# Optimization experiments

Measured on AMD Instinct MI355X. Metric: run time of the kernel, lower is better.

The kernel has to match this reference:

```python
import jax, jax.numpy as jnp
import numpy as np

HID, FFN, E, K = 1024, 4096, 8, 2
CAP_FACTOR = 1.25


def setup_inputs() -> dict:
    key = jax.random.key(0)
    k1, k2, k3, k4 = jax.random.split(key, 4)
    B, T = 4, 2048
    x = jax.random.normal(k1, (B, T, HID), dtype=jnp.float32)
    router_w = jax.random.normal(k2, (E, HID), dtype=jnp.float32) * 0.02
    w1 = jax.random.normal(k3, (E, HID, FFN), dtype=jnp.float32) * 0.02
    w2 = jax.random.normal(k4, (E, FFN, HID), dtype=jnp.float32) * 0.02
    return {"x": x, "router_w": router_w, "w1": w1, "w2": w2}


def reference(x, router_w, w1, w2):
    B, T, H = x.shape
    N = B * T
    x_flat = x.reshape(N, H)
    # capacity per expert (static, shape-derived)
    C = max(1, int(CAP_FACTOR * N / E * K))

    # router (eval mode: no noise)
    logits = x_flat @ router_w.T                      # [N, E]
    probs = jax.nn.softmax(logits, axis=-1)
    top_v, top_i = jax.lax.top_k(probs, K)            # [N, K]
    top_v = top_v / jnp.sum(top_v, axis=-1, keepdims=True)

    out = jnp.zeros_like(x_flat)
    for k in range(K):
        eid = top_i[:, k]                             # [N] expert id per token
        gate = top_v[:, k]                            # [N]
        # position of each token within its expert, in token order
        onehot = jax.nn.one_hot(eid, E, dtype=jnp.int32)          # [N, E]
        pos = jnp.take_along_axis(jnp.cumsum(onehot, axis=0), eid[:, None], axis=1)[:, 0] - 1
        keep = pos < C                                # capacity drop (first C in token order)
        slot = jnp.where(keep, eid * C + pos, E * C)  # dropped tokens -> dump slot

        # dispatch: scatter kept tokens into per-expert capacity buffers
        buf = jnp.zeros((E * C + 1, H), dtype=x.dtype).at[slot].add(
            x_flat * keep[:, None].astype(x.dtype))
        expert_in = buf[: E * C].reshape(E, C, H)     # [E, C, H]

        # per-expert FFN (grouped GEMM -> GELU -> grouped GEMM)
        h = jax.nn.gelu(jnp.einsum('ech,ehf->ecf', expert_in, w1), approximate=False)
        y = jnp.einsum('ecf,efh->ech', h, w2)         # [E, C, H]

        # combine: gather back to token order, mask dropped, apply gate
        tok = y.reshape(E * C, H)[jnp.minimum(slot, E * C - 1)]
        out = out + tok * (gate * keep.astype(x.dtype))[:, None]

    return out.reshape(B, T, H)
```

## Files before the change

### kernel.cpp

```cpp
#include <hip/hip_runtime.h>
#include <hip/hip_bf16.h>
#include <math.h>

#define N_TOK 8192
#define HIDD  1024
#define FFND  4096
#define NE    8
#define CAP   2560
#define TMX   20
#define TMX4  10
#define RMAX  16512

typedef __attribute__((ext_vector_type(4))) float  f32x4;
typedef __attribute__((ext_vector_type(8))) __bf16 bf16x8;

__device__ __forceinline__ unsigned short f2bf(float f) {
    unsigned u = __float_as_uint(f);
    u = (u + 0x7fffu + ((u >> 16) & 1u)) >> 16;
    return (unsigned short)u;
}

__device__ __forceinline__ void gld_lds16(const void* g, void* l) {
    __builtin_amdgcn_global_load_lds(
        (const __attribute__((address_space(1))) unsigned int*)g,
        (__attribute__((address_space(3))) unsigned int*)l, 16, 0, 0);
}

template <int R, int C>
__global__ __launch_bounds__(256) void transpose_cvt(const float* __restrict__ W,
                                                     unsigned short* __restrict__ Wt) {
    __shared__ unsigned short st[64][72];
    int e  = blockIdx.z;
    int r0 = blockIdx.y * 64, c0 = blockIdx.x * 64;
    int tid = threadIdx.x;
    int rb = tid >> 4, cq = tid & 15;
    const float* src = W + ((size_t)e * R + r0) * C + c0;
#pragma unroll
    for (int i = 0; i < 4; i++) {
        int kr = i * 16 + rb;
        float4 v = *reinterpret_cast<const float4*>(src + (size_t)kr * C + cq * 4);
        st[cq * 4 + 0][kr] = f2bf(v.x);
        st[cq * 4 + 1][kr] = f2bf(v.y);
        st[cq * 4 + 2][kr] = f2bf(v.z);
        st[cq * 4 + 3][kr] = f2bf(v.w);
    }
    __syncthreads();
    unsigned short* dst = Wt + ((size_t)e * C + c0) * R + r0;
#pragma unroll
    for (int i = 0; i < 4; i++) {
        int cr = i * 16 + rb;
        uint2 v = *reinterpret_cast<const uint2*>(&st[cr][cq * 4]);
        *reinterpret_cast<uint2*>(dst + (size_t)cr * R + cq * 4) = v;
    }
}

__global__ __launch_bounds__(256) void router_kernel(const float* __restrict__ x,
                                                     const float* __restrict__ rw,
                                                     unsigned short* __restrict__ xbf,
                                                     int* __restrict__ cnt,
                                                     int* __restrict__ tok,
                                                     float* __restrict__ gate) {
    __shared__ float4 rwl[2048];
    __shared__ int   e0s[32], e1s[32];
    __shared__ float g0s[32], g1s[32];
    __shared__ int   baseS[16];

    int tid = threadIdx.x, lane = tid & 63, w = tid >> 6;
    for (int i = tid; i < 2048; i += 256) rwl[i] = reinterpret_cast<const float4*>(rw)[i];
    __syncthreads();

    int tbase = blockIdx.x * 32 + w * 8;
    for (int i = 0; i < 8; i++) {
        int t = tbase + i;
        const float4* xr = reinterpret_cast<const float4*>(x) + (size_t)t * 256;
        float4 xv[4];
#pragma unroll
        for (int c = 0; c < 4; c++) xv[c] = xr[c * 64 + lane];
        uint2* xb = reinterpret_cast<uint2*>(xbf) + (size_t)t * 256;
#pragma unroll
        for (int c = 0; c < 4; c++) {
            uint2 p;
            p.x = (unsigned)f2bf(xv[c].x) | ((unsigned)f2bf(xv[c].y) << 16);
            p.y = (unsigned)f2bf(xv[c].z) | ((unsigned)f2bf(xv[c].w) << 16);
            xb[c * 64 + lane] = p;
        }
        float dot[NE];
#pragma unroll
        for (int e = 0; e < NE; e++) {
            float s = 0.f;
#pragma unroll
            for (int c = 0; c < 4; c++) {
                float4 a = rwl[e * 256 + c * 64 + lane];
                s += xv[c].x * a.x + xv[c].y * a.y + xv[c].z * a.z + xv[c].w * a.w;
            }
            dot[e] = s;
        }
#pragma unroll
        for (int e = 0; e < NE; e++) {
            float v = dot[e];
#pragma unroll
            for (int o = 32; o > 0; o >>= 1) v += __shfl_xor(v, o, 64);
            dot[e] = v;
        }
        if (lane == 0) {
            int e0 = 0; float l0 = dot[0];
#pragma unroll
            for (int e = 1; e < NE; e++) if (dot[e] > l0) { l0 = dot[e]; e0 = e; }
            int e1 = -1; float l1 = -3.4e38f;
#pragma unroll
            for (int e = 0; e < NE; e++) if (e != e0 && dot[e] > l1) { l1 = dot[e]; e1 = e; }
            float g0 = 1.f / (1.f + expf(l1 - l0));
            int j = w * 8 + i;
            e0s[j] = e0; e1s[j] = e1; g0s[j] = g0; g1s[j] = 1.f - g0;
        }
    }
    __syncthreads();

    int e0 = 255, e1 = 255, rank0 = 0, rank1 = 0, slotcnt = 0;
    float g0 = 0.f, g1 = 0.f;
    if (w == 0) {
        if (lane < 32) { e0 = e0s[lane]; e1 = e1s[lane]; g0 = g0s[lane]; g1 = g1s[lane]; }
        unsigned long long lt = (1ull << lane) - 1ull;
#pragma unroll
        for (int ee = 0; ee < NE; ee++) {
            unsigned long long m0 = __ballot(e0 == ee);
            unsigned long long m1 = __ballot(e1 == ee);
            if (e0 == ee) rank0 = (int)__popcll(m0 & lt);
            if (e1 == ee) rank1 = (int)__popcll(m1 & lt);
            if (lane == ee)      slotcnt = (int)__popcll(m0);
            if (lane == NE + ee) slotcnt = (int)__popcll(m1);
        }
        if (lane < 16) baseS[lane] = atomicAdd(&cnt[lane * 16], slotcnt);
    }
    __syncthreads();
    if (w == 0 && lane < 32) {
        int t = blockIdx.x * 32 + lane;
        int p0 = baseS[e0] + rank0;
        if (p0 < CAP) { tok[e0 * CAP + p0] = t; gate[e0 * CAP + p0] = g0; }
        int p1 = baseS[NE + e1] + rank1;
        if (p1 < CAP) { tok[(NE + e1) * CAP + p1] = t; gate[(NE + e1) * CAP + p1] = g1; }
    }
}

template <int KD, int ND, int KS, bool G1>
__global__ __launch_bounds__(512, 1) void ffn_gemm4p(const unsigned short* __restrict__ A,
                                                     const unsigned short* __restrict__ Bw,
                                                     unsigned short* __restrict__ H,
                                                     float* __restrict__ O,
                                                     const int* __restrict__ cntAll,
                                                     const int* __restrict__ tokL,
                                                     const float* __restrict__ gateL) {
    constexpr int TN    = ND / 256;
    constexpr int UNITS = TN * KS;
    constexpr int CH    = 4;
    constexpr int KDS   = KD / KS;
    constexpr int NT    = KDS / 32;
    constexpr int BUFSZ = 32768;

    extern __shared__ __align__(16) char smem[];

    int e = blockIdx.x & 7;
    int i = blockIdx.x >> 3;
    int cnt0 = min(cntAll[e * 16], CAP);
    int cnt1 = min(cntAll[(e + 8) * 16], CAP);
    int tmx0 = (cnt0 + 255) >> 8, tmx1 = (cnt1 + 255) >> 8;
    int tmsum = tmx0 + tmx1;
    if (tmsum == 0) return;
    int per_chunk = tmsum * CH;
    int c = i / per_chunk;
    if (c >= UNITS / CH) return;
    int r = i - c * per_chunk;
    int s, tm, cnt_e;
    if (r < tmx0 * CH) { s = e;     tm = r / CH; r -= tm * CH; cnt_e = cnt0; }
    else { r -= tmx0 * CH; s = e + 8; tm = r / CH; r -= tm * CH; cnt_e = cnt1; }
    int u  = c * CH + r;
    int tn = (KS > 1) ? (u / KS) : u;
    int ks = (KS > 1) ? (u % KS) : 0;

    int off_e = 0;
#pragma unroll
    for (int t = 0; t < 16; t++) off_e += (t < s) ? min(cntAll[t * 16], CAP) : 0;
    const int lbase = s * CAP;

    int tid = threadIdx.x;
    int l = tid & 63, w = tid >> 6;

    int rowi   = w * 16 + (l >> 2);
    int schunk = (((l & 3) ^ ((l >> 3) & 3)) << 4);

    int aoff[2], boff[2];
#pragma unroll
    for (int j = 0; j < 2; j++) {
        int p = tm * 256 + j * 128 + rowi;
        if (G1) {
            int t = tokL[lbase + (p < cnt_e ? p : 0)];
            aoff[j] = t * (KD * 2) + ks * (KDS * 2) + schunk;
        } else {
            aoff[j] = (off_e + p) * (KD * 2) + ks * (KDS * 2) + schunk;
        }
        int nr = e * ND + tn * 256 + j * 128 + rowi;
        boff[j] = nr * (KD * 2) + ks * (KDS * 2) + schunk;
    }
    int dstw = w * 1024;

    const char* Ab = (const char*)A;
    const char* Bb = (const char*)Bw;

    int wm = w >> 2, wn = w & 3;
    int rswz = (((l >> 4) ^ ((l >> 1) & 3)) << 4);
    int aRd = (wm * 128 + (l & 15)) * 64 + rswz;
    int bRd = (wn * 64 + (l & 15)) * 64 + rswz + 16384;

    f32x4 acc[8][4];
#pragma unroll
    for (int m = 0; m < 8; m++)
#pragma unroll
        for (int n = 0; n < 4; n++) acc[m][n] = (f32x4){0.f, 0.f, 0.f, 0.f};

#define STAGE_A4(bb) do { _Pragma("unroll") \
    for (int j = 0; j < 2; j++) { gld_lds16(Ab + aoff[j], smem + (bb) + j * 8192 + dstw); aoff[j] += 64; } } while (0)
#define STAGE_B4(bb) do { _Pragma("unroll") \
    for (int j = 0; j < 2; j++) { gld_lds16(Bb + boff[j], smem + (bb) + 16384 + j * 8192 + dstw); boff[j] += 64; } } while (0)

#pragma unroll
    for (int t = 0; t < 3; t++) { STAGE_A4(t * BUFSZ); STAGE_B4(t * BUFSZ); }
    asm volatile("s_waitcnt vmcnt(8)" ::: "memory");
    __builtin_amdgcn_s_barrier();
    asm volatile("" ::: "memory");

    for (int t = 0; t < NT; t++) {
        const int cb = (t & 3) * BUFSZ;
        const int nb = ((t + 3) & 3) * BUFSZ;
        bool pf = (t + 3) < NT;
        bf16x8 af[4], bf[4];
#pragma unroll
        for (int n = 0; n < 4; n++) bf[n] = *reinterpret_cast<const bf16x8*>(smem + cb + bRd + n * 1024);
#pragma unroll
        for (int m = 0; m < 4; m++) af[m] = *reinterpret_cast<const bf16x8*>(smem + cb + aRd + m * 1024);
        if (pf) STAGE_A4(nb);
        __builtin_amdgcn_s_barrier();
        asm volatile("" ::: "memory");
        asm volatile("s_waitcnt lgkmcnt(0)" ::: "memory");
        __builtin_amdgcn_sched_barrier(0);
        __builtin_amdgcn_s_setprio(1);
#pragma unroll
        for (int m = 0; m < 4; m++)
#pragma unroll
            for (int n = 0; n < 4; n++)
                acc[m][n] = __builtin_amdgcn_mfma_f32_16x16x32_bf16(af[m], bf[n], acc[m][n], 0, 0, 0);
        __builtin_amdgcn_s_setprio(0);
        __builtin_amdgcn_s_barrier();
        asm volatile("" ::: "memory");
#pragma unroll
        for (int m = 0; m < 4; m++) af[m] = *reinterpret_cast<const bf16x8*>(smem + cb + aRd + (m + 4) * 1024);
        if (pf) STAGE_B4(nb);
        if (t + 3 < NT)      asm volatile("s_waitcnt vmcnt(8)" ::: "memory");
        else if (t + 2 < NT) asm volatile("s_waitcnt vmcnt(4)" ::: "memory");
        else if (t + 1 < NT) asm volatile("s_waitcnt vmcnt(0)" ::: "memory");
        __builtin_amdgcn_s_barrier();
        asm volatile("" ::: "memory");
        asm volatile("s_waitcnt lgkmcnt(0)" ::: "memory");
        __builtin_amdgcn_sched_barrier(0);
        __builtin_amdgcn_s_setprio(1);
#pragma unroll
        for (int m = 0; m < 4; m++)
#pragma unroll
            for (int n = 0; n < 4; n++)
                acc[m + 4][n] = __builtin_amdgcn_mfma_f32_16x16x32_bf16(af[m], bf[n], acc[m + 4][n], 0, 0, 0);
        __builtin_amdgcn_s_setprio(0);
        __builtin_amdgcn_s_barrier();
        asm volatile("" ::: "memory");
    }
#undef STAGE_A4
#undef STAGE_B4

    if (G1) {
#pragma unroll
        for (int m = 0; m < 8; m++) {
#pragma unroll
            for (int j = 0; j < 4; j++) {
                int rr = wm * 128 + m * 16 + (l >> 4) * 4 + j;
                int p = tm * 256 + rr;
                if (p < cnt_e) {
                    unsigned short* hp = H + (size_t)(off_e + p) * ND + tn * 256 + wn * 64 + (l & 15);
#pragma unroll
                    for (int n = 0; n < 4; n++) {
                        float v = acc[m][n][j];
                        float g = 0.5f * v * (1.f + erff(v * 0.70710678118654752f));
                        hp[n * 16] = f2bf(g);
                    }
                }
            }
        }
    } else {
#pragma unroll
        for (int m = 0; m < 8; m++) {
#pragma unroll
            for (int j = 0; j < 4; j++) {
                int rr = wm * 128 + m * 16 + (l >> 4) * 4 + j;
                int p = tm * 256 + rr;
                if (p < cnt_e) {
                    int t = tokL[lbase + p];
                    float gv = gateL[lbase + p];
                    float* op = O + (size_t)t * ND + tn * 256 + wn * 64 + (l & 15);
#pragma unroll
                    for (int n = 0; n < 4; n++) atomicAdd(op + n * 16, gv * acc[m][n][j]);
                }
            }
        }
    }
}

template <int KD, int ND, bool G1>
__global__ __launch_bounds__(256) void ffn_gemm(const unsigned short* __restrict__ A,
                                                const float* __restrict__ W,
                                                unsigned short* __restrict__ H,
                                                float* __restrict__ O,
                                                const int* __restrict__ cntAll,
                                                const int* __restrict__ tokL,
                                                const float* __restrict__ gateL,
                                                int slot0, int pbase) {
    constexpr int TN = ND / 128;
    int bid = blockIdx.x;
    int tn  = bid % TN;
    int tme = bid / TN;
    int tm  = tme % TMX;
    int s   = slot0 + tme / TMX;
    int eW  = s & 7;
    int cnt_e = min(cntAll[s * 16], CAP);
    if (tm * 128 >= cnt_e) return;
    int off_e = 0;
#pragma unroll
    for (int i = 0; i < 16; i++) {
        int c = min(cntAll[i * 16], CAP);
        off_e += (i >= pbase && i < s) ? c : 0;
    }
    const int lbase = s * CAP;

    __shared__ __align__(16) unsigned short At[128 * 32];
    __shared__ __align__(16) unsigned short Bt[128 * 32];

    int tid = threadIdx.x;
    int w = tid >> 6, l = tid & 63;
    int wr = w >> 1, wc = w & 1;

    int r1 = tid >> 2, q1 = tid & 3;
    int r2 = r1 + 64;
    const char* aSrc1;
    const char* aSrc2;
    if (G1) {
        int p1 = tm * 128 + r1, p2 = tm * 128 + r2;
        int t1 = tokL[lbase + (p1 < cnt_e ? p1 : 0)];
        int t2 = tokL[lbase + (p2 < cnt_e ? p2 : 0)];
        aSrc1 = (const char*)(A + (size_t)t1 * KD) + ((q1 ^ ((r1 >> 1) & 3)) << 4);
        aSrc2 = (const char*)(A + (size_t)t2 * KD) + ((q1 ^ ((r2 >> 1) & 3)) << 4);
    } else {
        size_t row1 = (size_t)off_e + tm * 128 + r1;
        size_t row2 = row1 + 64;
        aSrc1 = (const char*)(A + row1 * KD) + ((q1 ^ ((r1 >> 1) & 3)) << 4);
        aSrc2 = (const char*)(A + row2 * KD) + ((q1 ^ ((r2 >> 1) & 3)) << 4);
    }
    char* aDst1 = (char*)At + w * 1024;
    char* aDst2 = aDst1 + 4096;

    const float* bSrc[4];
    int bOff[16];
#pragma unroll
    for (int j = 0; j < 4; j++) {
        int fidx = j * 1024 + tid * 4;
        int kk = fidx >> 7, n = fidx & 127;
        bSrc[j] = W + (size_t)eW * KD * ND + (size_t)kk * ND + tn * 128 + n;
#pragma unroll
        for (int i = 0; i < 4; i++) {
            int nn = n + i;
            bOff[j * 4 + i] = nn * 64 + ((((kk >> 3) ^ ((nn >> 1) & 3))) << 4) + ((kk & 7) << 1);
        }
    }

    int aro[4], bro[4];
#pragma unroll
    for (int m = 0; m < 4; m++) {
        int rr = wr * 64 + m * 16 + (l & 15);
        aro[m] = rr * 64 + (((l >> 4) ^ ((rr >> 1) & 3)) << 4);
        int cc = wc * 64 + m * 16 + (l & 15);
        bro[m] = cc * 64 + (((l >> 4) ^ ((cc >> 1) & 3)) << 4);
    }

    f32x4 zf = {0.f, 0.f, 0.f, 0.f};
    f32x4 acc[4][4];
#pragma unroll
    for (int m = 0; m < 4; m++)
#pragma unroll
        for (int n = 0; n < 4; n++) acc[m][n] = zf;

    for (int k0 = 0; k0 < KD; k0 += 32) {
        gld_lds16(aSrc1 + (size_t)k0 * 2, aDst1);
        gld_lds16(aSrc2 + (size_t)k0 * 2, aDst2);
        float4 bv[4];
#pragma unroll
        for (int j = 0; j < 4; j++) bv[j] = *reinterpret_cast<const float4*>(bSrc[j] + (size_t)k0 * ND);
        char* btc = (char*)Bt;
#pragma unroll
        for (int j = 0; j < 4; j++) {
            *(unsigned short*)(btc + bOff[j * 4 + 0]) = f2bf(bv[j].x);
            *(unsigned short*)(btc + bOff[j * 4 + 1]) = f2bf(bv[j].y);
            *(unsigned short*)(btc + bOff[j * 4 + 2]) = f2bf(bv[j].z);
            *(unsigned short*)(btc + bOff[j * 4 + 3]) = f2bf(bv[j].w);
        }
        __syncthreads();
        bf16x8 af[4], bf[4];
#pragma unroll
        for (int m = 0; m < 4; m++) af[m] = *reinterpret_cast<const bf16x8*>((const char*)At + aro[m]);
#pragma unroll
        for (int n = 0; n < 4; n++) bf[n] = *reinterpret_cast<const bf16x8*>((const char*)Bt + bro[n]);
#pragma unroll
        for (int m = 0; m < 4; m++)
#pragma unroll
            for (int n = 0; n < 4; n++)
                acc[m][n] = __builtin_amdgcn_mfma_f32_16x16x32_bf16(af[m], bf[n], acc[m][n], 0, 0, 0);
        __syncthreads();
    }

    if (G1) {
#pragma unroll
        for (int m = 0; m < 4; m++) {
#pragma unroll
            for (int j = 0; j < 4; j++) {
                int rr = wr * 64 + m * 16 + (l >> 4) * 4 + j;
                int p = tm * 128 + rr;
                if (p < cnt_e) {
                    size_t row = (size_t)(off_e + p);
                    unsigned short* hp = H + row * ND + tn * 128 + wc * 64 + (l & 15);
#pragma unroll
                    for (int n = 0; n < 4; n++) {
                        float v = acc[m][n][j];
                        float g = 0.5f * v * (1.f + erff(v * 0.70710678118654752f));
                        hp[n * 16] = f2bf(g);
                    }
                }
            }
        }
    } else {
#pragma unroll
        for (int m = 0; m < 4; m++) {
#pragma unroll
            for (int j = 0; j < 4; j++) {
                int rr = wr * 64 + m * 16 + (l >> 4) * 4 + j;
                int p = tm * 128 + rr;
                if (p < cnt_e) {
                    int t = tokL[lbase + p];
                    float gv = gateL[lbase + p];
                    float* op = O + (size_t)t * ND + tn * 128 + wc * 64 + (l & 15);
#pragma unroll
                    for (int n = 0; n < 4; n++) atomicAdd(op + n * 16, gv * acc[m][n][j]);
                }
            }
        }
    }
}

extern "C" void kernel_launch(void* const* d_in, const int* in_sizes, int n_in,
                              void* d_out, int out_size, void* d_ws, size_t ws_size,
                              hipStream_t stream) {
    const float* x  = (const float*)d_in[0];
    const float* rw = (const float*)d_in[1];
    const float* w1 = (const float*)d_in[2];
    const float* w2 = (const float*)d_in[3];
    float* out = (float*)d_out;
    char* ws = (char*)d_ws;

    int*   cnt  = (int*)ws;
    int*   tok  = (int*)(ws + 4096);
    float* gate = (float*)(ws + 4096 + 16 * CAP * 4);
    unsigned short* xbf = (unsigned short*)(ws + (1 << 20));
    size_t hOff = (1 << 20) + (size_t)N_TOK * HIDD * 2;
    unsigned short* h = (unsigned short*)(ws + hOff);

    size_t w1tSz = (size_t)NE * HIDD * FFND * 2;
    size_t hBig = (size_t)RMAX * FFND * 2;
    size_t needBig = hOff + hBig + 2 * w1tSz;

    hipMemsetAsync(cnt, 0, 1024, stream);
    hipMemsetAsync(d_out, 0, (size_t)N_TOK * HIDD * 4, stream);

    hipLaunchKernelGGL(router_kernel, dim3(N_TOK / 32), dim3(256), 0, stream,
                       x, rw, xbf, cnt, tok, gate);

    if (ws_size >= needBig) {
        unsigned short* w1t = (unsigned short*)(ws + hOff + hBig);
        unsigned short* w2t = (unsigned short*)(ws + hOff + hBig + w1tSz);
        hipLaunchKernelGGL((transpose_cvt<HIDD, FFND>), dim3(FFND / 64, HIDD / 64, NE), dim3(256), 0, stream, w1, w1t);
        hipLaunchKernelGGL((transpose_cvt<FFND, HIDD>), dim3(HIDD / 64, FFND / 64, NE), dim3(256), 0, stream, w2, w2t);
        constexpr int SMEM = 4 * 32768;
        hipLaunchKernelGGL((ffn_gemm4p<HIDD, FFND, 1, true>), dim3(8 * 2 * TMX4 * 16), dim3(512),
                           SMEM, stream, xbf, w1t, h, (float*)nullptr, cnt, tok, gate);
        hipLaunchKernelGGL((ffn_gemm4p<FFND, HIDD, 2, false>), dim3(8 * 2 * TMX4 * 8), dim3(512),
                           SMEM, stream, h, w2t, (unsigned short*)nullptr, out, cnt, tok, gate);
    } else {
        for (int k = 0; k < 2; k++) {
            hipLaunchKernelGGL((ffn_gemm<HIDD, FFND, true>), dim3(8 * TMX * (FFND / 128)), dim3(256), 0, stream,
                               xbf, w1, h, (float*)nullptr, cnt, tok, gate, 8 * k, 8 * k);
            hipLaunchKernelGGL((ffn_gemm<FFND, HIDD, false>), dim3(8 * TMX * (HIDD / 128)), dim3(256), 0, stream,
                               h, w2, (unsigned short*)nullptr, out, cnt, tok, gate, 8 * k, 8 * k);
        }
    }
}
```

Measured before the change: 604.4 us.

## Make expert GEMMs persistent with BK=64 tiles and split A/B staging rings

Replaces the one-tile-per-block grid with a persistent grid of 256 blocks, each looping over its expert's tiles with stride 32. The K step doubles to 64 and uses new LDS swizzles. Staging is split into a triple-buffered A ring and a double-buffered B ring, with loads interleaved across four MFMA phases. The aim is to cut launch and tail overhead and halve loop and barrier count per K element. In exchange LDS grows to 160KB per block, and the static stride-32 tile split can leave blocks unevenly loaded.

Result: faster. 558.9 us (-7.5%).

```diff
diff --git a/kernel.cpp b/kernel.cpp
--- a/kernel.cpp
+++ b/kernel.cpp
@@ -8,7 +8,6 @@
 #define NE    8
 #define CAP   2560
 #define TMX   20
-#define TMX4  10
 #define RMAX  16512
 
 typedef __attribute__((ext_vector_type(4))) float  f32x4;
@@ -143,7 +142,7 @@
 }
 
 template <int KD, int ND, int KS, bool G1>
-__global__ __launch_bounds__(512, 1) void ffn_gemm4p(const unsigned short* __restrict__ A,
+__global__ __launch_bounds__(512, 1) void ffn_gemm_t(const unsigned short* __restrict__ A_,
                                                      const unsigned short* __restrict__ Bw,
                                                      unsigned short* __restrict__ H,
                                                      float* __restrict__ O,
@@ -151,164 +150,222 @@
                                                      const int* __restrict__ tokL,
                                                      const float* __restrict__ gateL) {
     constexpr int TN    = ND / 256;
-    constexpr int UNITS = TN * KS;
-    constexpr int CH    = 4;
+    constexpr int TNKS  = TN * KS;
     constexpr int KDS   = KD / KS;
-    constexpr int NT    = KDS / 32;
-    constexpr int BUFSZ = 32768;
+    constexpr int NT    = KDS / 64;
+    constexpr int ABUF  = 32768;
+    constexpr int BBASE = 3 * ABUF;
+    constexpr int BBUF  = 32768;
 
     extern __shared__ __align__(16) char smem[];
 
-    int e = blockIdx.x & 7;
-    int i = blockIdx.x >> 3;
+    int e = blockIdx.x & 7, pb = blockIdx.x >> 3;
     int cnt0 = min(cntAll[e * 16], CAP);
     int cnt1 = min(cntAll[(e + 8) * 16], CAP);
     int tmx0 = (cnt0 + 255) >> 8, tmx1 = (cnt1 + 255) >> 8;
     int tmsum = tmx0 + tmx1;
     if (tmsum == 0) return;
-    int per_chunk = tmsum * CH;
-    int c = i / per_chunk;
-    if (c >= UNITS / CH) return;
-    int r = i - c * per_chunk;
-    int s, tm, cnt_e;
-    if (r < tmx0 * CH) { s = e;     tm = r / CH; r -= tm * CH; cnt_e = cnt0; }
-    else { r -= tmx0 * CH; s = e + 8; tm = r / CH; r -= tm * CH; cnt_e = cnt1; }
-    int u  = c * CH + r;
-    int tn = (KS > 1) ? (u / KS) : u;
-    int ks = (KS > 1) ? (u % KS) : 0;
-
-    int off_e = 0;
-#pragma unroll
-    for (int t = 0; t < 16; t++) off_e += (t < s) ? min(cntAll[t * 16], CAP) : 0;
-    const int lbase = s * CAP;
-
-    int tid = threadIdx.x;
-    int l = tid & 63, w = tid >> 6;
-
-    int rowi   = w * 16 + (l >> 2);
-    int schunk = (((l & 3) ^ ((l >> 3) & 3)) << 4);
-
-    int aoff[2], boff[2];
-#pragma unroll
-    for (int j = 0; j < 2; j++) {
-        int p = tm * 256 + j * 128 + rowi;
-        if (G1) {
-            int t = tokL[lbase + (p < cnt_e ? p : 0)];
-            aoff[j] = t * (KD * 2) + ks * (KDS * 2) + schunk;
-        } else {
-            aoff[j] = (off_e + p) * (KD * 2) + ks * (KDS * 2) + schunk;
-        }
-        int nr = e * ND + tn * 256 + j * 128 + rowi;
-        boff[j] = nr * (KD * 2) + ks * (KDS * 2) + schunk;
-    }
-    int dstw = w * 1024;
-
-    const char* Ab = (const char*)A;
+    int offA = 0, offB = 0;
+#pragma unroll
+    for (int t = 0; t < 16; t++) {
+        int cc = min(cntAll[t * 16], CAP);
+        if (t < e)     offA += cc;
+        if (t < e + 8) offB += cc;
+    }
+    int total = tmsum * TNKS;
+
+    int tid = threadIdx.x, l = tid & 63, w = tid >> 6;
+    int wm = w >> 2, wn = w & 3;
+
+    int srow = tid >> 3, sch = tid & 7;
+    int swzb = ((sch ^ (srow & 7)) << 4);
+    int dstL = tid * 16;
+
+    int c0 = ((((l >> 4)    ) ^ (l & 7)) << 4);
+    int c1 = ((((l >> 4) + 4) ^ (l & 7)) << 4);
+    int aBaseRd = wm * 16384 + (l & 15) * 128;
+    int bBaseRd = (wn >> 1) * 16384 + (wn & 1) * 8192 + (l & 15) * 128;
+
+    const char* Ab = (const char*)A_;
     const char* Bb = (const char*)Bw;
 
-    int wm = w >> 2, wn = w & 3;
-    int rswz = (((l >> 4) ^ ((l >> 1) & 3)) << 4);
-    int aRd = (wm * 128 + (l & 15)) * 64 + rswz;
-    int bRd = (wn * 64 + (l & 15)) * 64 + rswz + 16384;
-
-    f32x4 acc[8][4];
-#pragma unroll
-    for (int m = 0; m < 8; m++)
-#pragma unroll
-        for (int n = 0; n < 4; n++) acc[m][n] = (f32x4){0.f, 0.f, 0.f, 0.f};
-
-#define STAGE_A4(bb) do { _Pragma("unroll") \
-    for (int j = 0; j < 2; j++) { gld_lds16(Ab + aoff[j], smem + (bb) + j * 8192 + dstw); aoff[j] += 64; } } while (0)
-#define STAGE_B4(bb) do { _Pragma("unroll") \
-    for (int j = 0; j < 2; j++) { gld_lds16(Bb + boff[j], smem + (bb) + 16384 + j * 8192 + dstw); boff[j] += 64; } } while (0)
-
-#pragma unroll
-    for (int t = 0; t < 3; t++) { STAGE_A4(t * BUFSZ); STAGE_B4(t * BUFSZ); }
-    asm volatile("s_waitcnt vmcnt(8)" ::: "memory");
-    __builtin_amdgcn_s_barrier();
-    asm volatile("" ::: "memory");
-
-    for (int t = 0; t < NT; t++) {
-        const int cb = (t & 3) * BUFSZ;
-        const int nb = ((t + 3) & 3) * BUFSZ;
-        bool pf = (t + 3) < NT;
-        bf16x8 af[4], bf[4];
-#pragma unroll
-        for (int n = 0; n < 4; n++) bf[n] = *reinterpret_cast<const bf16x8*>(smem + cb + bRd + n * 1024);
-#pragma unroll
-        for (int m = 0; m < 4; m++) af[m] = *reinterpret_cast<const bf16x8*>(smem + cb + aRd + m * 1024);
-        if (pf) STAGE_A4(nb);
+#define STG_A(h, bi) do{ \
+    gld_lds16(Ab + aof[h][0], smem + (bi)*ABUF + (h)*16384 + dstL);        aof[h][0] += 128; \
+    gld_lds16(Ab + aof[h][1], smem + (bi)*ABUF + (h)*16384 + 8192 + dstL); aof[h][1] += 128; }while(0)
+#define STG_B(h, bi) do{ \
+    gld_lds16(Bb + bof[h][0], smem + BBASE + (bi)*BBUF + (h)*16384 + dstL);        bof[h][0] += 128; \
+    gld_lds16(Bb + bof[h][1], smem + BBASE + (bi)*BBUF + (h)*16384 + 8192 + dstL); bof[h][1] += 128; }while(0)
+
+    for (int u0 = pb; u0 < total; u0 += 32) {
+        int tnks = u0 / tmsum, tmi = u0 - tnks * tmsum;
+        int s, tm, cnt_e, off_e;
+        if (tmi < tmx0) { s = e;     tm = tmi;        cnt_e = cnt0; off_e = offA; }
+        else            { s = e + 8; tm = tmi - tmx0; cnt_e = cnt1; off_e = offB; }
+        int tn, ks;
+        if (KS > 1) { tn = tnks >> 1; ks = tnks & 1; } else { tn = tnks; ks = 0; }
+        const int lbase = s * CAP;
+
+        int aof[2][2], bof[2][2];
+#pragma unroll
+        for (int h = 0; h < 2; h++)
+#pragma unroll
+            for (int sw2 = 0; sw2 < 2; sw2++) {
+                int p = tm * 256 + h * 128 + sw2 * 64 + srow;
+                int rowg;
+                if (G1) rowg = tokL[lbase + (p < cnt_e ? p : 0)];
+                else    rowg = off_e + p;
+                aof[h][sw2] = rowg * (KD * 2) + ks * (KDS * 2) + swzb;
+                int nr = e * ND + tn * 256 + h * 128 + sw2 * 64 + srow;
+                bof[h][sw2] = nr * (KD * 2) + ks * (KDS * 2) + swzb;
+            }
+
+        f32x4 acc[8][4];
+#pragma unroll
+        for (int m = 0; m < 8; m++)
+#pragma unroll
+            for (int n = 0; n < 4; n++) acc[m][n] = (f32x4){0.f, 0.f, 0.f, 0.f};
+
+        STG_A(0, 0); STG_A(1, 0); STG_B(0, 0); STG_B(1, 0); STG_A(0, 1); STG_A(1, 1);
+        asm volatile("s_waitcnt vmcnt(4)" ::: "memory");
         __builtin_amdgcn_s_barrier();
         asm volatile("" ::: "memory");
-        asm volatile("s_waitcnt lgkmcnt(0)" ::: "memory");
-        __builtin_amdgcn_sched_barrier(0);
-        __builtin_amdgcn_s_setprio(1);
-#pragma unroll
-        for (int m = 0; m < 4; m++)
-#pragma unroll
-            for (int n = 0; n < 4; n++)
-                acc[m][n] = __builtin_amdgcn_mfma_f32_16x16x32_bf16(af[m], bf[n], acc[m][n], 0, 0, 0);
-        __builtin_amdgcn_s_setprio(0);
-        __builtin_amdgcn_s_barrier();
-        asm volatile("" ::: "memory");
-#pragma unroll
-        for (int m = 0; m < 4; m++) af[m] = *reinterpret_cast<const bf16x8*>(smem + cb + aRd + (m + 4) * 1024);
-        if (pf) STAGE_B4(nb);
-        if (t + 3 < NT)      asm volatile("s_waitcnt vmcnt(8)" ::: "memory");
-        else if (t + 2 < NT) asm volatile("s_waitcnt vmcnt(4)" ::: "memory");
-        else if (t + 1 < NT) asm volatile("s_waitcnt vmcnt(0)" ::: "memory");
-        __builtin_amdgcn_s_barrier();
-        asm volatile("" ::: "memory");
-        asm volatile("s_waitcnt lgkmcnt(0)" ::: "memory");
-        __builtin_amdgcn_sched_barrier(0);
-        __builtin_amdgcn_s_setprio(1);
-#pragma unroll
-        for (int m = 0; m < 4; m++)
-#pragma unroll
-            for (int n = 0; n < 4; n++)
-                acc[m + 4][n] = __builtin_amdgcn_mfma_f32_16x16x32_bf16(af[m], bf[n], acc[m + 4][n], 0, 0, 0);
-        __builtin_amdgcn_s_setprio(0);
-        __builtin_amdgcn_s_barrier();
-        asm volatile("" ::: "memory");
-    }
-#undef STAGE_A4
-#undef STAGE_B4
-
-    if (G1) {
-#pragma unroll
-        for (int m = 0; m < 8; m++) {
-#pragma unroll
-            for (int j = 0; j < 4; j++) {
-                int rr = wm * 128 + m * 16 + (l >> 4) * 4 + j;
-                int p = tm * 256 + rr;
-                if (p < cnt_e) {
-                    unsigned short* hp = H + (size_t)(off_e + p) * ND + tn * 256 + wn * 64 + (l & 15);
-#pragma unroll
-                    for (int n = 0; n < 4; n++) {
-                        float v = acc[m][n][j];
-                        float g = 0.5f * v * (1.f + erff(v * 0.70710678118654752f));
-                        hp[n * 16] = f2bf(g);
+
+        int ia = 0, ib = 0;
+        for (int t = 0; t < NT; t++) {
+            const char* bA = smem + ia * ABUF;
+            const char* bB = smem + BBASE + ib * BBUF;
+            int ian = ia + 2; if (ian >= 3) ian -= 3;
+            int ibn = ib ^ 1;
+            bool stB = (t + 1 < NT), stA = (t + 2 < NT);
+            bf16x8 af[4][2], b01[2][2], b23[2][2];
+
+#pragma unroll
+            for (int m = 0; m < 4; m++) {
+                af[m][0] = *reinterpret_cast<const bf16x8*>(bA + aBaseRd + m * 2048 + c0);
+                af[m][1] = *reinterpret_cast<const bf16x8*>(bA + aBaseRd + m * 2048 + c1);
+            }
+#pragma unroll
+            for (int n = 0; n < 2; n++) {
+                b01[n][0] = *reinterpret_cast<const bf16x8*>(bB + bBaseRd + n * 2048 + c0);
+                b01[n][1] = *reinterpret_cast<const bf16x8*>(bB + bBaseRd + n * 2048 + c1);
+            }
+            if (stB) STG_B(0, ibn);
+            __builtin_amdgcn_s_barrier();
+            asm volatile("s_waitcnt lgkmcnt(0)" ::: "memory");
+            __builtin_amdgcn_sched_barrier(0);
+            __builtin_amdgcn_s_setprio(1);
+#pragma unroll
+            for (int m = 0; m < 4; m++)
+#pragma unroll
+                for (int n = 0; n < 2; n++) {
+                    acc[m][n] = __builtin_amdgcn_mfma_f32_16x16x32_bf16(af[m][0], b01[n][0], acc[m][n], 0, 0, 0);
+                    acc[m][n] = __builtin_amdgcn_mfma_f32_16x16x32_bf16(af[m][1], b01[n][1], acc[m][n], 0, 0, 0);
+                }
+            __builtin_amdgcn_s_setprio(0);
+            __builtin_amdgcn_s_barrier();
+            asm volatile("" ::: "memory");
+
+#pragma unroll
+            for (int n = 0; n < 2; n++) {
+                b23[n][0] = *reinterpret_cast<const bf16x8*>(bB + bBaseRd + (n + 2) * 2048 + c0);
+                b23[n][1] = *reinterpret_cast<const bf16x8*>(bB + bBaseRd + (n + 2) * 2048 + c1);
+            }
+            if (stB) STG_B(1, ibn);
+            __builtin_amdgcn_s_barrier();
+            asm volatile("s_waitcnt lgkmcnt(0)" ::: "memory");
+            __builtin_amdgcn_sched_barrier(0);
+            __builtin_amdgcn_s_setprio(1);
+#pragma unroll
+            for (int m = 0; m < 4; m++)
+#pragma unroll
+                for (int n = 0; n < 2; n++) {
+                    acc[m][n + 2] = __builtin_amdgcn_mfma_f32_16x16x32_bf16(af[m][0], b23[n][0], acc[m][n + 2], 0, 0, 0);
+                    acc[m][n + 2] = __builtin_amdgcn_mfma_f32_16x16x32_bf16(af[m][1], b23[n][1], acc[m][n + 2], 0, 0, 0);
+                }
+            __builtin_amdgcn_s_setprio(0);
+            __builtin_amdgcn_s_barrier();
+            asm volatile("" ::: "memory");
+
+#pragma unroll
+            for (int m = 0; m < 4; m++) {
+                af[m][0] = *reinterpret_cast<const bf16x8*>(bA + aBaseRd + 8192 + m * 2048 + c0);
+                af[m][1] = *reinterpret_cast<const bf16x8*>(bA + aBaseRd + 8192 + m * 2048 + c1);
+            }
+            if (stA) STG_A(0, ian);
+            __builtin_amdgcn_s_barrier();
+            asm volatile("s_waitcnt lgkmcnt(0)" ::: "memory");
+            __builtin_amdgcn_sched_barrier(0);
+            __builtin_amdgcn_s_setprio(1);
+#pragma unroll
+            for (int m = 0; m < 4; m++)
+#pragma unroll
+                for (int n = 0; n < 2; n++) {
+                    acc[m + 4][n + 2] = __builtin_amdgcn_mfma_f32_16x16x32_bf16(af[m][0], b23[n][0], acc[m + 4][n + 2], 0, 0, 0);
+                    acc[m + 4][n + 2] = __builtin_amdgcn_mfma_f32_16x16x32_bf16(af[m][1], b23[n][1], acc[m + 4][n + 2], 0, 0, 0);
+                }
+            __builtin_amdgcn_s_setprio(0);
+            __builtin_amdgcn_s_barrier();
+            asm volatile("" ::: "memory");
+
+            if (stA) STG_A(1, ian);
+            if (stA)      { asm volatile("s_waitcnt vmcnt(4)" ::: "memory"); }
+            else if (stB) { asm volatile("s_waitcnt vmcnt(0)" ::: "memory"); }
+            __builtin_amdgcn_s_barrier();
+            asm volatile("" ::: "memory");
+            __builtin_amdgcn_s_setprio(1);
+#pragma unroll
+            for (int m = 0; m < 4; m++)
+#pragma unroll
+                for (int n = 0; n < 2; n++) {
+                    acc[m + 4][n] = __builtin_amdgcn_mfma_f32_16x16x32_bf16(af[m][0], b01[n][0], acc[m + 4][n], 0, 0, 0);
+                    acc[m + 4][n] = __builtin_amdgcn_mfma_f32_16x16x32_bf16(af[m][1], b01[n][1], acc[m + 4][n], 0, 0, 0);
+                }
+            __builtin_amdgcn_s_setprio(0);
+            __builtin_amdgcn_s_barrier();
+            asm volatile("" ::: "memory");
+
+            ia = (ia + 1 == 3) ? 0 : ia + 1;
+            ib ^= 1;
+        }
+
+        if (G1) {
+#pragma unroll
+            for (int m = 0; m < 8; m++) {
+#pragma unroll
+                for (int j = 0; j < 4; j++) {
+                    int rr = wm * 128 + m * 16 + (l >> 4) * 4 + j;
+                    int p = tm * 256 + rr;
+                    if (p < cnt_e) {
+                        unsigned short* hp = H + (size_t)(off_e + p) * ND + tn * 256 + wn * 64 + (l & 15);
+#pragma unroll
+                        for (int n = 0; n < 4; n++) {
+                            float v = acc[m][n][j];
+                            float g = 0.5f * v * (1.f + erff(v * 0.70710678118654752f));
+                            hp[n * 16] = f2bf(g);
+                        }
                     }
                 }
             }
-        }
-    } else {
-#pragma unroll
-        for (int m = 0; m < 8; m++) {
-#pragma unroll
-            for (int j = 0; j < 4; j++) {
-                int rr = wm * 128 + m * 16 + (l >> 4) * 4 + j;
-                int p = tm * 256 + rr;
-                if (p < cnt_e) {
-                    int t = tokL[lbase + p];
-                    float gv = gateL[lbase + p];
-                    float* op = O + (size_t)t * ND + tn * 256 + wn * 64 + (l & 15);
-#pragma unroll
-                    for (int n = 0; n < 4; n++) atomicAdd(op + n * 16, gv * acc[m][n][j]);
-                }
-            }
-        }
-    }
+        } else {
+#pragma unroll
+            for (int m = 0; m < 8; m++) {
+#pragma unroll
+                for (int j = 0; j < 4; j++) {
+                    int rr = wm * 128 + m * 16 + (l >> 4) * 4 + j;
+                    int p = tm * 256 + rr;
+                    if (p < cnt_e) {
+                        int t = tokL[lbase + p];
+                        float gv = gateL[lbase + p];
+                        float* op = O + (size_t)t * ND + tn * 256 + wn * 64 + (l & 15);
+#pragma unroll
+                        for (int n = 0; n < 4; n++) atomicAdd(op + n * 16, gv * acc[m][n][j]);
+                    }
+                }
+            }
+        }
+    }
+#undef STG_A
+#undef STG_B
 }
 
 template <int KD, int ND, bool G1>
@@ -491,11 +548,16 @@
         unsigned short* w2t = (unsigned short*)(ws + hOff + hBig + w1tSz);
         hipLaunchKernelGGL((transpose_cvt<HIDD, FFND>), dim3(FFND / 64, HIDD / 64, NE), dim3(256), 0, stream, w1, w1t);
         hipLaunchKernelGGL((transpose_cvt<FFND, HIDD>), dim3(HIDD / 64, FFND / 64, NE), dim3(256), 0, stream, w2, w2t);
-        constexpr int SMEM = 4 * 32768;
-        hipLaunchKernelGGL((ffn_gemm4p<HIDD, FFND, 1, true>), dim3(8 * 2 * TMX4 * 16), dim3(512),
-                           SMEM, stream, xbf, w1t, h, (float*)nullptr, cnt, tok, gate);
-        hipLaunchKernelGGL((ffn_gemm4p<FFND, HIDD, 2, false>), dim3(8 * 2 * TMX4 * 8), dim3(512),
-                           SMEM, stream, h, w2t, (unsigned short*)nullptr, out, cnt, tok, gate);
+
+        constexpr int SMEM = 5 * 32768;
+        hipFuncSetAttribute((const void*)&ffn_gemm_t<HIDD, FFND, 1, true>,
+                            hipFuncAttributeMaxDynamicSharedMemorySize, SMEM);
+        hipFuncSetAttribute((const void*)&ffn_gemm_t<FFND, HIDD, 2, false>,
+                            hipFuncAttributeMaxDynamicSharedMemorySize, SMEM);
+        hipLaunchKernelGGL((ffn_gemm_t<HIDD, FFND, 1, true>), dim3(256), dim3(512), SMEM, stream,
+                           xbf, w1t, h, (float*)nullptr, cnt, tok, gate);
+        hipLaunchKernelGGL((ffn_gemm_t<FFND, HIDD, 2, false>), dim3(256), dim3(512), SMEM, stream,
+                           h, w2t, (unsigned short*)nullptr, out, cnt, tok, gate);
     } else {
         for (int k = 0; k < 2; k++) {
             hipLaunchKernelGGL((ffn_gemm<HIDD, FFND, true>), dim3(8 * TMX * (FFND / 128)), dim3(256), 0, stream,
```
